# Kernel optimization log

Hardware: AMD Instinct MI355X
Metric: run time of the kernel (lower is better)

## Reference

```python
import jax, jax.numpy as jnp
import numpy as np

N_WINDOWS = 4
WIN_H, WIN_W = 512, 512          # module 'size'
IMG_H, IMG_W = 1024, 1024        # 2x2 tiling of windows
N_MASKS = 32                     # n_windows * masks_per_window
MPW = N_MASKS // N_WINDOWS       # 8 masks per window (channel 0 of each block = background)
SLOT_DIM = 64
SIM_THRESH = 0.1                 # module 'similarity'


def setup_inputs() -> dict:
    key = jax.random.key(0)
    k1, k2 = jax.random.split(key)
    masks = jax.random.normal(k1, (1, N_MASKS, IMG_H, IMG_W), dtype=jnp.float32)
    slot_features = jax.random.normal(k2, (N_WINDOWS, MPW - 1, SLOT_DIM), dtype=jnp.float32)
    # static window layout, equivalent to keys ['w_0_0','w_512_0','w_0_512','w_512_512']
    pad_left = jnp.array([0, WIN_W, 0, WIN_W], dtype=jnp.int32)
    pad_top = jnp.array([0, 0, WIN_H, WIN_H], dtype=jnp.int32)
    return {"masks": masks, "slot_features": slot_features,
            "pad_left": pad_left, "pad_top": pad_top}


def _merge_windows(masks, slot_features, pl, pt):
    """pl, pt: python int lists (static metadata parsed from keys)."""
    B, C, H, W = masks.shape
    mpw = C // N_WINDOWS

    # --- to_one_hot: argmax over channel dim, one-hot back to [B,C,H,W] float ---
    ids = jnp.argmax(masks, axis=1)                                   # [B,H,W]
    m = jnp.moveaxis(jax.nn.one_hot(ids, C, dtype=masks.dtype), -1, 1)  # [B,C,H,W]

    ranges = [(i * mpw, (i + 1) * mpw) for i in range(N_WINDOWS)]

    # --- adjacency over window pads (static) ---
    adjacency = []
    for i in range(N_WINDOWS):
        for j in range(i + 1, N_WINDOWS):
            if pt[i] == pt[j] and abs(pl[i] - pl[j]) == WIN_W:
                adjacency.append((i, j, True) if pl[i] < pl[j] else (j, i, True))
            if pl[i] == pl[j] and abs(pt[i] - pt[j]) == WIN_H:
                adjacency.append((i, j, False) if pt[i] < pt[j] else (j, i, False))

    # --- per-channel edge-touch booleans (vectorized replacement of set building) ---
    edge_l = jnp.zeros((C,), bool)
    edge_r = jnp.zeros((C,), bool)
    edge_t = jnp.zeros((C,), bool)
    edge_b = jnp.zeros((C,), bool)
    for wi, (s, e) in enumerate(ranges):
        ys, ye = max(pt[wi], 0), min(pt[wi] + WIN_H, H)
        xs, xe = max(pl[wi], 0), min(pl[wi] + WIN_W, W)
        if ys >= ye or xs >= xe:
            continue
        win = m[0, s:e, ys:ye, xs:xe]                # [mpw, hh, ww]
        edge_l = edge_l.at[s:e].set(jnp.any(win[:, :, 0] == 1, axis=-1))
        edge_r = edge_r.at[s:e].set(jnp.any(win[:, :, -1] == 1, axis=-1))
        edge_t = edge_t.at[s:e].set(jnp.any(win[:, 0, :] == 1, axis=-1))
        edge_b = edge_b.at[s:e].set(jnp.any(win[:, -1, :] == 1, axis=-1))

    # --- static candidate pair list (background channels ci % mpw == 0 excluded) ---
    ci_l, cj_l, wi_l, wj_l, hz_l = [], [], [], [], []
    for wi, wj, horiz in adjacency:
        si, ei = ranges[wi]
        sj, ej = ranges[wj]
        for ci in range(si + 1, ei):
            for cj in range(sj + 1, ej):
                ci_l.append(ci); cj_l.append(cj)
                wi_l.append(wi); wj_l.append(wj); hz_l.append(horiz)
    P = len(ci_l)
    if P == 0:
        return m

    ci_a = jnp.array(ci_l, jnp.int32)
    cj_a = jnp.array(cj_l, jnp.int32)
    horiz = jnp.array(hz_l)

    # --- cosine similarities for all pairs at once ---
    sf_n = slot_features / (jnp.linalg.norm(slot_features, axis=-1, keepdims=True) + 1e-8)
    rel_i = np.array(ci_l) % mpw - 1
    rel_j = np.array(cj_l) % mpw - 1
    fi = sf_n[np.array(wi_l), rel_i]                 # [P, D]
    fj = sf_n[np.array(wj_l), rel_j]
    sims = jnp.sum(fi * fj, axis=-1)                 # [P]

    edge_ok = jnp.where(horiz, edge_r[ci_a] & edge_l[cj_a], edge_b[ci_a] & edge_t[cj_a])
    passing = edge_ok & (sims > SIM_THRESH)          # [P]

    # --- sequential dedup/merge scan (order-dependent, like the torch loop) ---
    def step(carry, xs):
        m, merged = carry
        ci, cj, ok = xs
        cond = ok & ~merged[ci] & ~merged[cj]
        keep = jnp.minimum(ci, cj)
        rem = jnp.maximum(ci, cj)
        rem_ch = jnp.take(m, rem, axis=1)            # [B,H,W]
        m = m.at[:, keep].add(jnp.where(cond, rem_ch, 0.0))
        m = m.at[:, rem].set(jnp.where(cond, jnp.zeros_like(rem_ch), rem_ch))
        merged = merged.at[rem].set(merged[rem] | cond)
        return (m, merged), None

    (m, _), _ = jax.lax.scan(step, (m, jnp.zeros((C,), bool)), (ci_a, cj_a, passing))
    return m


def reference(masks, slot_features, pad_left, pad_top):
    # pads encode the (static) window layout parsed from the string keys
    pl = [int(v) for v in np.asarray(pad_left)]
    pt = [int(v) for v in np.asarray(pad_top)]
    return _merge_windows(masks, slot_features, pl, pt)
```

## Files before the change

### kernel.cpp

```cpp
#include <hip/hip_runtime.h>

#define IMG_H 1024
#define IMG_W 1024
#define NPIX (IMG_H * IMG_W)
#define N_MASKS 32
#define N_WINDOWS 4
#define MPW 8
#define WIN_H 512
#define WIN_W 512
#define SIM_THRESH 0.1f

#define NBLK 256
#define PXB  4096

typedef float vf4 __attribute__((ext_vector_type(4)));

#define WS_EDGE  0
#define WS_IDS   (NBLK * 16)

__global__ __launch_bounds__(256) void k_argmax(const float* __restrict__ masks,
                                                const int* __restrict__ pl,
                                                const int* __restrict__ pt,
                                                uint4* __restrict__ edge_blocks,
                                                unsigned char* __restrict__ ids) {
    __shared__ int spl[4], spt[4];
    __shared__ unsigned sem[4];
    const int tid = threadIdx.x;
    if (tid < 4) { spl[tid] = pl[tid]; spt[tid] = pt[tid]; sem[tid] = 0u; }
    __syncthreads();

    const int wave = tid >> 6;
    const int lane = tid & 63;
    const int base = blockIdx.x * PXB + wave * 1024 + lane * 4;

    float bv[16];
    int   bc[16];
#pragma unroll
    for (int k = 0; k < 4; k++) {
        const vf4 v = __builtin_nontemporal_load((const vf4*)(masks + base + k * 256));
        bv[4*k+0] = v.x; bv[4*k+1] = v.y; bv[4*k+2] = v.z; bv[4*k+3] = v.w;
        bc[4*k+0] = 0;   bc[4*k+1] = 0;   bc[4*k+2] = 0;   bc[4*k+3] = 0;
    }
#pragma unroll
    for (int c = 1; c < N_MASKS; c++) {
        const float* mc = masks + (size_t)c * NPIX + base;
#pragma unroll
        for (int k = 0; k < 4; k++) {
            const vf4 v = __builtin_nontemporal_load((const vf4*)(mc + k * 256));
            if (v.x > bv[4*k+0]) { bv[4*k+0] = v.x; bc[4*k+0] = c; }
            if (v.y > bv[4*k+1]) { bv[4*k+1] = v.y; bc[4*k+1] = c; }
            if (v.z > bv[4*k+2]) { bv[4*k+2] = v.z; bc[4*k+2] = c; }
            if (v.w > bv[4*k+3]) { bv[4*k+3] = v.w; bc[4*k+3] = c; }
        }
    }
#pragma unroll
    for (int k = 0; k < 4; k++)
        *(uchar4*)(ids + base + k * 256) =
            make_uchar4((unsigned char)bc[4*k+0], (unsigned char)bc[4*k+1],
                        (unsigned char)bc[4*k+2], (unsigned char)bc[4*k+3]);

#pragma unroll
    for (int k = 0; k < 4; k++) {
        const int px = base + k * 256;
        const int y  = px >> 10;
        const int x0 = px & (IMG_W - 1);
#pragma unroll
        for (int wi = 0; wi < N_WINDOWS; wi++) {
            const int xs = max(spl[wi], 0), xe = min(spl[wi] + WIN_W, IMG_W);
            const int ys = max(spt[wi], 0), ye = min(spt[wi] + WIN_H, IMG_H);
            if (ys >= ye || xs >= xe) continue;
            if (y < ys || y >= ye) continue;
#pragma unroll
            for (int j = 0; j < 4; j++) {
                const int x = x0 + j;
                if (x < xs || x >= xe) continue;
                const int c = bc[4*k+j];
                if ((c >> 3) != wi) continue;
                const unsigned bit = 1u << c;
                if (x == xs)     atomicOr(&sem[0], bit);
                if (x == xe - 1) atomicOr(&sem[1], bit);
                if (y == ys)     atomicOr(&sem[2], bit);
                if (y == ye - 1) atomicOr(&sem[3], bit);
            }
        }
    }
    __syncthreads();
    if (tid == 0) edge_blocks[blockIdx.x] = make_uint4(sem[0], sem[1], sem[2], sem[3]);
}

__global__ __launch_bounds__(256) void k_merge_write(const unsigned char* __restrict__ ids,
                                                     const float* __restrict__ sf,
                                                     const int* __restrict__ pl,
                                                     const int* __restrict__ pt,
                                                     const uint4* __restrict__ edge_blocks,
                                                     float* __restrict__ out) {
    __shared__ float sfn[28 * 65];
    __shared__ unsigned step_word[512];
    __shared__ uint4 wred[4];
    __shared__ unsigned fedge[4];
    __shared__ int sP;
    __shared__ int loc[32];

    const int tid = threadIdx.x;
    const int lane = tid & 63;
    const int wave = tid >> 6;

    unsigned el = 0, er = 0, et = 0, eb = 0;
    for (int b = tid; b < NBLK; b += 256) {
        const uint4 w = edge_blocks[b];
        el |= w.x; er |= w.y; et |= w.z; eb |= w.w;
    }
#pragma unroll
    for (int off = 1; off < 64; off <<= 1) {
        el |= __shfl_xor(el, off);
        er |= __shfl_xor(er, off);
        et |= __shfl_xor(et, off);
        eb |= __shfl_xor(eb, off);
    }
    if (lane == 0) wred[wave] = make_uint4(el, er, et, eb);

#pragma unroll
    for (int i = 0; i < 7; i++) {
        const int r = wave + 4 * i;
        const float v = sf[r * 64 + lane];
        float s = v * v;
#pragma unroll
        for (int off = 1; off < 64; off <<= 1) s += __shfl_xor(s, off);
        sfn[r * 65 + lane] = v * (1.0f / (sqrtf(s) + 1e-8f));
    }
    __syncthreads();

    if (tid == 0) {
        unsigned fl = wred[0].x | wred[1].x | wred[2].x | wred[3].x;
        unsigned fr = wred[0].y | wred[1].y | wred[2].y | wred[3].y;
        unsigned ft = wred[0].z | wred[1].z | wred[2].z | wred[3].z;
        unsigned fb = wred[0].w | wred[1].w | wred[2].w | wred[3].w;
        fedge[0] = fl; fedge[1] = fr; fedge[2] = ft; fedge[3] = fb;

        int lpl[4], lpt[4];
        for (int i = 0; i < 4; i++) { lpl[i] = pl[i]; lpt[i] = pt[i]; }
        int aI[8], aJ[8], aH[8], na = 0;
        for (int i = 0; i < N_WINDOWS; i++)
            for (int j = i + 1; j < N_WINDOWS; j++) {
                if (lpt[i] == lpt[j] && abs(lpl[i] - lpl[j]) == WIN_W) {
                    if (lpl[i] < lpl[j]) { aI[na] = i; aJ[na] = j; }
                    else                 { aI[na] = j; aJ[na] = i; }
                    aH[na] = 1; na++;
                }
                if (lpl[i] == lpl[j] && abs(lpt[i] - lpt[j]) == WIN_H) {
                    if (lpt[i] < lpt[j]) { aI[na] = i; aJ[na] = j; }
                    else                 { aI[na] = j; aJ[na] = i; }
                    aH[na] = 0; na++;
                }
            }
        int P = 0;
        for (int a = 0; a < na; a++)
            for (int ci = aI[a] * MPW + 1; ci < (aI[a] + 1) * MPW; ci++)
                for (int cj = aJ[a] * MPW + 1; cj < (aJ[a] + 1) * MPW; cj++)
                    step_word[P++] = (unsigned)ci | ((unsigned)cj << 8)
                                   | ((unsigned)aH[a] << 16);
        sP = P;
    }
    __syncthreads();

    const int P = sP;
    {
        const unsigned ger = fedge[1], gel = fedge[0], geb = fedge[3], get = fedge[2];
        for (int p = tid; p < P; p += 256) {
            const unsigned w = step_word[p];
            const int ci = w & 255, cj = (w >> 8) & 255, hz = (w >> 16) & 1;
            const float* fi = &sfn[((ci >> 3) * (MPW - 1) + (ci & 7) - 1) * 65];
            const float* fj = &sfn[((cj >> 3) * (MPW - 1) + (cj & 7) - 1) * 65];
            float s = 0.f;
#pragma unroll
            for (int k = 0; k < 64; k++) s += fi[k] * fj[k];
            const bool eok = hz ? (((ger >> ci) & 1u) && ((gel >> cj) & 1u))
                                : (((geb >> ci) & 1u) && ((get >> cj) & 1u));
            if (eok && s > SIM_THRESH) step_word[p] = w | (1u << 17);
        }
    }
    __syncthreads();

    if (wave == 0) {
        unsigned merged = 0;
        int myloc = lane;
        for (int p = 0; p < P; p++) {
            const unsigned w = step_word[p];
            if (w >> 17) {
                const int ci = w & 255, cj = (w >> 8) & 255;
                if (!((merged >> ci) & 1u) && !((merged >> cj) & 1u)) {
                    const int keep = min(ci, cj), rem = max(ci, cj);
                    if (myloc == rem) myloc = keep;
                    merged |= 1u << rem;
                }
            }
        }
        if (lane < 32) loc[lane] = myloc;
    }
    __syncthreads();

    const int base = blockIdx.x * PXB + wave * 1024 + lane * 4;
    int r[16];
#pragma unroll
    for (int k = 0; k < 4; k++) {
        const uchar4 id4 = *(const uchar4*)(ids + base + k * 256);
        r[4*k+0] = loc[id4.x]; r[4*k+1] = loc[id4.y];
        r[4*k+2] = loc[id4.z]; r[4*k+3] = loc[id4.w];
    }
#pragma unroll
    for (int c = 0; c < N_MASKS; c++) {
        float* oc = out + (size_t)c * NPIX + base;
#pragma unroll
        for (int k = 0; k < 4; k++) {
            vf4 v;
            v.x = (r[4*k+0] == c) ? 1.0f : 0.0f;
            v.y = (r[4*k+1] == c) ? 1.0f : 0.0f;
            v.z = (r[4*k+2] == c) ? 1.0f : 0.0f;
            v.w = (r[4*k+3] == c) ? 1.0f : 0.0f;
            __builtin_nontemporal_store(v, (vf4*)(oc + k * 256));
        }
    }
}

extern "C" void kernel_launch(void* const* d_in, const int* in_sizes, int n_in,
                              void* d_out, int out_size, void* d_ws, size_t ws_size,
                              hipStream_t stream) {
    const float* masks = (const float*)d_in[0];
    const float* sf    = (const float*)d_in[1];
    const int*   pl    = (const int*)d_in[2];
    const int*   pt    = (const int*)d_in[3];
    float* out = (float*)d_out;

    char* ws = (char*)d_ws;
    uint4* edge_blocks = (uint4*)(ws + WS_EDGE);
    unsigned char* ids = (unsigned char*)(ws + WS_IDS);

    k_argmax<<<NBLK, 256, 0, stream>>>(masks, pl, pt, edge_blocks, ids);
    k_merge_write<<<NBLK, 256, 0, stream>>>(ids, sf, pl, pt, edge_blocks, out);
}
```

Before: 255.5 us.

## Fuse argmax and merge-write into one kernel with a grid-wide atomic barrier

```diff
diff --git a/kernel.cpp b/kernel.cpp
--- a/kernel.cpp
+++ b/kernel.cpp
@@ -15,22 +15,32 @@
 
 typedef float vf4 __attribute__((ext_vector_type(4)));
 
-#define WS_EDGE  0
-#define WS_IDS   (NBLK * 16)
-
-__global__ __launch_bounds__(256) void k_argmax(const float* __restrict__ masks,
-                                                const int* __restrict__ pl,
-                                                const int* __restrict__ pt,
-                                                uint4* __restrict__ edge_blocks,
-                                                unsigned char* __restrict__ ids) {
+#define WS_EDGE 0
+#define WS_CNT  (NBLK * 16)
+
+__global__ __launch_bounds__(256) void k_fused(const float* __restrict__ masks,
+                                               const float* __restrict__ sf,
+                                               const int* __restrict__ pl,
+                                               const int* __restrict__ pt,
+                                               uint4* __restrict__ edge_blocks,
+                                               unsigned* __restrict__ cnt,
+                                               float* __restrict__ out) {
     __shared__ int spl[4], spt[4];
     __shared__ unsigned sem[4];
+    __shared__ float sfn[28 * 65];
+    __shared__ unsigned step_word[512];
+    __shared__ uint4 wred[4];
+    __shared__ unsigned fedge[4];
+    __shared__ int sP;
+    __shared__ int loc[32];
+
     const int tid = threadIdx.x;
+    const int lane = tid & 63;
+    const int wave = tid >> 6;
+
     if (tid < 4) { spl[tid] = pl[tid]; spt[tid] = pt[tid]; sem[tid] = 0u; }
     __syncthreads();
 
-    const int wave = tid >> 6;
-    const int lane = tid & 63;
     const int base = blockIdx.x * PXB + wave * 1024 + lane * 4;
 
     float bv[16];
@@ -53,11 +63,6 @@
             if (v.w > bv[4*k+3]) { bv[4*k+3] = v.w; bc[4*k+3] = c; }
         }
     }
-#pragma unroll
-    for (int k = 0; k < 4; k++)
-        *(uchar4*)(ids + base + k * 256) =
-            make_uchar4((unsigned char)bc[4*k+0], (unsigned char)bc[4*k+1],
-                        (unsigned char)bc[4*k+2], (unsigned char)bc[4*k+3]);
 
 #pragma unroll
     for (int k = 0; k < 4; k++) {
@@ -84,40 +89,6 @@
             }
         }
     }
-    __syncthreads();
-    if (tid == 0) edge_blocks[blockIdx.x] = make_uint4(sem[0], sem[1], sem[2], sem[3]);
-}
-
-__global__ __launch_bounds__(256) void k_merge_write(const unsigned char* __restrict__ ids,
-                                                     const float* __restrict__ sf,
-                                                     const int* __restrict__ pl,
-                                                     const int* __restrict__ pt,
-                                                     const uint4* __restrict__ edge_blocks,
-                                                     float* __restrict__ out) {
-    __shared__ float sfn[28 * 65];
-    __shared__ unsigned step_word[512];
-    __shared__ uint4 wred[4];
-    __shared__ unsigned fedge[4];
-    __shared__ int sP;
-    __shared__ int loc[32];
-
-    const int tid = threadIdx.x;
-    const int lane = tid & 63;
-    const int wave = tid >> 6;
-
-    unsigned el = 0, er = 0, et = 0, eb = 0;
-    for (int b = tid; b < NBLK; b += 256) {
-        const uint4 w = edge_blocks[b];
-        el |= w.x; er |= w.y; et |= w.z; eb |= w.w;
-    }
-#pragma unroll
-    for (int off = 1; off < 64; off <<= 1) {
-        el |= __shfl_xor(el, off);
-        er |= __shfl_xor(er, off);
-        et |= __shfl_xor(et, off);
-        eb |= __shfl_xor(eb, off);
-    }
-    if (lane == 0) wred[wave] = make_uint4(el, er, et, eb);
 
 #pragma unroll
     for (int i = 0; i < 7; i++) {
@@ -131,14 +102,12 @@
     __syncthreads();
 
     if (tid == 0) {
-        unsigned fl = wred[0].x | wred[1].x | wred[2].x | wred[3].x;
-        unsigned fr = wred[0].y | wred[1].y | wred[2].y | wred[3].y;
-        unsigned ft = wred[0].z | wred[1].z | wred[2].z | wred[3].z;
-        unsigned fb = wred[0].w | wred[1].w | wred[2].w | wred[3].w;
-        fedge[0] = fl; fedge[1] = fr; fedge[2] = ft; fedge[3] = fb;
+        edge_blocks[blockIdx.x] = make_uint4(sem[0], sem[1], sem[2], sem[3]);
+        __threadfence();
+        atomicAdd(cnt, 1u);
 
         int lpl[4], lpt[4];
-        for (int i = 0; i < 4; i++) { lpl[i] = pl[i]; lpt[i] = pt[i]; }
+        for (int i = 0; i < 4; i++) { lpl[i] = spl[i]; lpt[i] = spt[i]; }
         int aI[8], aJ[8], aH[8], na = 0;
         for (int i = 0; i < N_WINDOWS; i++)
             for (int j = i + 1; j < N_WINDOWS; j++) {
@@ -164,19 +133,56 @@
     __syncthreads();
 
     const int P = sP;
+    for (int p = tid; p < P; p += 256) {
+        const unsigned w = step_word[p];
+        const int ci = w & 255, cj = (w >> 8) & 255;
+        const float* fi = &sfn[((ci >> 3) * (MPW - 1) + (ci & 7) - 1) * 65];
+        const float* fj = &sfn[((cj >> 3) * (MPW - 1) + (cj & 7) - 1) * 65];
+        float s = 0.f;
+#pragma unroll
+        for (int k = 0; k < 64; k++) s += fi[k] * fj[k];
+        if (s > SIM_THRESH) step_word[p] = w | (1u << 18);
+    }
+    __syncthreads();
+
+    if (tid == 0) {
+        while (__hip_atomic_load(cnt, __ATOMIC_RELAXED, __HIP_MEMORY_SCOPE_AGENT) < NBLK)
+            __builtin_amdgcn_s_sleep(2);
+        __threadfence();
+    }
+    __syncthreads();
+
     {
-        const unsigned ger = fedge[1], gel = fedge[0], geb = fedge[3], get = fedge[2];
+        const uint4 w = edge_blocks[tid];
+        unsigned el = w.x, er = w.y, et = w.z, eb = w.w;
+#pragma unroll
+        for (int off = 1; off < 64; off <<= 1) {
+            el |= __shfl_xor(el, off);
+            er |= __shfl_xor(er, off);
+            et |= __shfl_xor(et, off);
+            eb |= __shfl_xor(eb, off);
+        }
+        if (lane == 0) wred[wave] = make_uint4(el, er, et, eb);
+    }
+    __syncthreads();
+    if (tid == 0) {
+        fedge[0] = wred[0].x | wred[1].x | wred[2].x | wred[3].x;
+        fedge[1] = wred[0].y | wred[1].y | wred[2].y | wred[3].y;
+        fedge[2] = wred[0].z | wred[1].z | wred[2].z | wred[3].z;
+        fedge[3] = wred[0].w | wred[1].w | wred[2].w | wred[3].w;
+    }
+    __syncthreads();
+
+    {
+        const unsigned gel = fedge[0], ger = fedge[1], get = fedge[2], geb = fedge[3];
         for (int p = tid; p < P; p += 256) {
             const unsigned w = step_word[p];
-            const int ci = w & 255, cj = (w >> 8) & 255, hz = (w >> 16) & 1;
-            const float* fi = &sfn[((ci >> 3) * (MPW - 1) + (ci & 7) - 1) * 65];
-            const float* fj = &sfn[((cj >> 3) * (MPW - 1) + (cj & 7) - 1) * 65];
-            float s = 0.f;
-#pragma unroll
-            for (int k = 0; k < 64; k++) s += fi[k] * fj[k];
-            const bool eok = hz ? (((ger >> ci) & 1u) && ((gel >> cj) & 1u))
-                                : (((geb >> ci) & 1u) && ((get >> cj) & 1u));
-            if (eok && s > SIM_THRESH) step_word[p] = w | (1u << 17);
+            if ((w >> 18) & 1u) {
+                const int ci = w & 255, cj = (w >> 8) & 255, hz = (w >> 16) & 1;
+                const bool eok = hz ? (((ger >> ci) & 1u) && ((gel >> cj) & 1u))
+                                    : (((geb >> ci) & 1u) && ((get >> cj) & 1u));
+                if (eok) step_word[p] = w | (1u << 17);
+            }
         }
     }
     __syncthreads();
@@ -186,7 +192,7 @@
         int myloc = lane;
         for (int p = 0; p < P; p++) {
             const unsigned w = step_word[p];
-            if (w >> 17) {
+            if ((w >> 17) & 1u) {
                 const int ci = w & 255, cj = (w >> 8) & 255;
                 if (!((merged >> ci) & 1u) && !((merged >> cj) & 1u)) {
                     const int keep = min(ci, cj), rem = max(ci, cj);
@@ -199,14 +205,9 @@
     }
     __syncthreads();
 
-    const int base = blockIdx.x * PXB + wave * 1024 + lane * 4;
     int r[16];
 #pragma unroll
-    for (int k = 0; k < 4; k++) {
-        const uchar4 id4 = *(const uchar4*)(ids + base + k * 256);
-        r[4*k+0] = loc[id4.x]; r[4*k+1] = loc[id4.y];
-        r[4*k+2] = loc[id4.z]; r[4*k+3] = loc[id4.w];
-    }
+    for (int i = 0; i < 16; i++) r[i] = loc[bc[i]];
 #pragma unroll
     for (int c = 0; c < N_MASKS; c++) {
         float* oc = out + (size_t)c * NPIX + base;
@@ -233,8 +234,8 @@
 
     char* ws = (char*)d_ws;
     uint4* edge_blocks = (uint4*)(ws + WS_EDGE);
-    unsigned char* ids = (unsigned char*)(ws + WS_IDS);
-
-    k_argmax<<<NBLK, 256, 0, stream>>>(masks, pl, pt, edge_blocks, ids);
-    k_merge_write<<<NBLK, 256, 0, stream>>>(ids, sf, pl, pt, edge_blocks, out);
+    unsigned* cnt = (unsigned*)(ws + WS_CNT);
+
+    hipMemsetAsync(cnt, 0, sizeof(unsigned), stream);
+    k_fused<<<NBLK, 256, 0, stream>>>(masks, sf, pl, pt, edge_blocks, cnt, out);
 }
```

New measurement: 250.7 us. About the same (-1.9%).
